# Kernel optimization log

Hardware: AMD Instinct MI355X
Metric: run time of the kernel (lower is better)

The kernel has to match this reference:

```python
import jax, jax.numpy as jnp
import numpy as np

B, N, M = 8, 4096, 4096
CHAMFER_W, EMD_W, UNC_W = 1.0, 0.5, 0.01


def setup_inputs() -> dict:
    key = jax.random.key(0)
    k1, k2, k3 = jax.random.split(key, 3)
    return {
        "pred_pc": jax.random.normal(k1, (B, N, 3), dtype=jnp.float32),
        "target_pc": jax.random.normal(k2, (B, M, 3), dtype=jnp.float32),
        "uncertainty": jax.random.uniform(k3, (B, N), dtype=jnp.float32),
    }


def reference(pred_pc, target_pc, uncertainty):
    # squared pairwise distances via ||p||^2 + ||t||^2 - 2 p.t  -> [B, N, M]
    pred_sq = jnp.sum(pred_pc ** 2, axis=2, keepdims=True)            # [B, N, 1]
    tgt_sq = jnp.sum(target_pc ** 2, axis=2, keepdims=True)           # [B, M, 1]
    cross = jnp.einsum('bnd,bmd->bnm', pred_pc, target_pc)            # [B, N, M]
    d2 = pred_sq + jnp.swapaxes(tgt_sq, 1, 2) - 2.0 * cross           # [B, N, M]

    # ChamferDistanceLoss: mean of min squared dists both directions
    chamfer = jnp.mean(jnp.min(d2, axis=2)) + jnp.mean(jnp.min(d2, axis=1))

    # EMDLoss: torch.cdist p=2 (euclidean), min over targets, mean
    dist = jnp.sqrt(jnp.clip(d2, 0.0))
    emd = jnp.mean(jnp.min(dist, axis=2))

    # uncertainty regularizer
    unc_reg = jnp.mean(uncertainty) * UNC_W

    total = chamfer * CHAMFER_W + emd * EMD_W + unc_reg
    return total
```

## Files before the change

kernel.cpp:

```cpp
#include <hip/hip_runtime.h>
#include <math.h>

typedef _Float16 half8  __attribute__((ext_vector_type(8)));
typedef float    f32x16 __attribute__((ext_vector_type(16)));

#define Bb 8
#define Nn 4096
#define Mm 4096
#define BLOCK 256
#define WAVES 4
#define NTA 2
#define QBLK 256
#define TBLK 1024
#define MT (TBLK / 32)
#define MS 4
#define QTILES (Nn / QBLK)
#define NQ (2 * Bb * Nn)

template<int CTRL>
__device__ __forceinline__ float dppmin(float v) {
    int iv = __float_as_int(v);
    iv = __builtin_amdgcn_update_dpp(iv, iv, CTRL, 0xF, 0xF, false);
    return fminf(v, __int_as_float(iv));
}
__device__ __forceinline__ float rowmin32(float v) {
    v = dppmin<0xB1>(v);
    v = dppmin<0x4E>(v);
    v = dppmin<0x141>(v);
    v = dppmin<0x140>(v);
    v = fminf(v, __shfl_xor(v, 16));
    return v;
}


__global__ void __launch_bounds__(BLOCK) chamfer_mfma32_kernel(
    const float* __restrict__ pred,
    const float* __restrict__ targ,
    float* __restrict__ mins)
{
    __shared__ uint4 fragB[TBLK];

    const int tid  = threadIdx.x;
    const int lane = tid & 63;
    const int wave = tid >> 6;

    const int id  = blockIdx.x;
    const int ms  = id & 3;
    const int qt  = (id >> 2) & 15;
    const int b   = (id >> 6) & 7;
    const int dir = id >> 9;

    const float* Q = dir ? targ : pred;
    const float* T = dir ? pred : targ;

    for (int s = tid; s < TBLK; s += BLOCK) {
        const float* gp = T + ((size_t)b * Mm + ms * TBLK + s) * 3;
        _Float16 xh = (_Float16)gp[0], yh = (_Float16)gp[1], zh = (_Float16)gp[2];
        float xq = (float)xh, yq = (float)yh, zq = (float)zh;
        float tt = fmaf(xq, xq, fmaf(yq, yq, zq * zq));
        _Float16 th = (_Float16)tt;
        _Float16 tl = (_Float16)(tt - (float)th);
        const _Float16 m2 = (_Float16)(-2.0f);
        half8 h;
        h[0] = m2 * xh; h[1] = m2 * yh; h[2] = m2 * zh; h[3] = (_Float16)1.0f;
        h[4] = th; h[5] = (_Float16)1.0f; h[6] = tl; h[7] = (_Float16)0.0f;
        fragB[s] = *reinterpret_cast<uint4*>(&h);
    }

    const int qbase = qt * QBLK + wave * (NTA * 32);
    half8 a0, a1;
    #pragma unroll
    for (int e = 0; e < 8; ++e) { a0[e] = (_Float16)0.0f; a1[e] = (_Float16)0.0f; }
    if (lane < 32) {
        #pragma unroll
        for (int t = 0; t < NTA; ++t) {
            const int n = qbase + t * 32 + lane;
            const float* gp = Q + ((size_t)b * Nn + n) * 3;
            _Float16 xh = (_Float16)gp[0], yh = (_Float16)gp[1], zh = (_Float16)gp[2];
            float xq = (float)xh, yq = (float)yh, zq = (float)zh;
            float pp = fmaf(xq, xq, fmaf(yq, yq, zq * zq));
            _Float16 ph = (_Float16)pp;
            _Float16 pl = (_Float16)(pp - (float)ph);
            half8 h;
            h[0] = xh; h[1] = yh; h[2] = zh; h[3] = ph;
            h[4] = (_Float16)1.0f; h[5] = pl; h[6] = (_Float16)1.0f; h[7] = (_Float16)0.0f;
            if (t == 0) a0 = h; else a1 = h;
        }
    }
    __syncthreads();

    const int col = lane & 31;
    const f32x16 cz = {};
    const float inf = __builtin_inff();
    f32x16 acc0, acc1;
    #pragma unroll
    for (int k = 0; k < 16; ++k) { acc0[k] = inf; acc1[k] = inf; }

    for (int j = 0; j < MT; j += 2) {
        half8 b0 = *reinterpret_cast<const half8*>(&fragB[(j << 5) + col]);
        half8 b1 = *reinterpret_cast<const half8*>(&fragB[((j + 1) << 5) + col]);
        f32x16 c0 = __builtin_amdgcn_mfma_f32_32x32x16_f16(a0, b0, cz, 0, 0, 0);
        f32x16 c1 = __builtin_amdgcn_mfma_f32_32x32x16_f16(a0, b1, cz, 0, 0, 0);
        #pragma unroll
        for (int k = 0; k < 16; ++k)
            acc0[k] = fminf(fminf(acc0[k], c0[k]), c1[k]);
        f32x16 d0 = __builtin_amdgcn_mfma_f32_32x32x16_f16(a1, b0, cz, 0, 0, 0);
        f32x16 d1 = __builtin_amdgcn_mfma_f32_32x32x16_f16(a1, b1, cz, 0, 0, 0);
        #pragma unroll
        for (int k = 0; k < 16; ++k)
            acc1[k] = fminf(fminf(acc1[k], d0[k]), d1[k]);
    }

    const int hi = lane >> 5;
    const size_t qoff = ((size_t)dir * Bb + b) * Nn;
    #pragma unroll
    for (int r = 0; r < 16; ++r) {
        float v0 = rowmin32(acc0[r]);
        float v1 = rowmin32(acc1[r]);
        if (col == 0) {
            const int rl = (r & 3) + 8 * (r >> 2) + 4 * hi;
            const size_t q0 = qoff + qbase + rl;
            mins[q0 * MS + ms]        = v0;
            mins[(q0 + 32) * MS + ms] = v1;
        }
    }
}

__global__ void __launch_bounds__(256) reduce_kernel(
    const float* __restrict__ mins, const float* __restrict__ unc,
    float* __restrict__ partials)
{
    const int q = blockIdx.x * 256 + threadIdx.x;
    const float4* m4 = (const float4*)mins;

    float4 a4 = m4[q];
    float4 b4 = m4[q + 32768];
    float vA = fminf(fminf(a4.x, a4.y), fminf(a4.z, a4.w));
    float vB = fminf(fminf(b4.x, b4.y), fminf(b4.z, b4.w));
    float sA = vA, sE = sqrtf(fmaxf(vA, 0.f)), sB = vB, sU = unc[q];

    #pragma unroll
    for (int off = 32; off > 0; off >>= 1) {
        sA += __shfl_down(sA, off);  sE += __shfl_down(sE, off);
        sB += __shfl_down(sB, off);  sU += __shfl_down(sU, off);
    }
    __shared__ float sw[4][4];
    const int lane = threadIdx.x & 63, wave = threadIdx.x >> 6;
    if (lane == 0) { sw[wave][0] = sA; sw[wave][1] = sE;
                     sw[wave][2] = sB; sw[wave][3] = sU; }
    __syncthreads();
    if (threadIdx.x < 4) {
        partials[blockIdx.x * 4 + threadIdx.x] =
            sw[0][threadIdx.x] + sw[1][threadIdx.x] +
            sw[2][threadIdx.x] + sw[3][threadIdx.x];
    }
}

__global__ void __launch_bounds__(64) finalize_kernel(
    const float* __restrict__ partials, float* __restrict__ out)
{
    const float4* p4 = (const float4*)partials;
    float4 s0 = p4[threadIdx.x], s1 = p4[threadIdx.x + 64];
    float sA = s0.x + s1.x, sE = s0.y + s1.y, sB = s0.z + s1.z, sU = s0.w + s1.w;
    #pragma unroll
    for (int off = 32; off > 0; off >>= 1) {
        sA += __shfl_down(sA, off);  sE += __shfl_down(sE, off);
        sB += __shfl_down(sB, off);  sU += __shfl_down(sU, off);
    }
    if (threadIdx.x == 0) {
        const float invBN = 1.0f / (float)(Bb * Nn);
        const float invBM = 1.0f / (float)(Bb * Mm);
        out[0] = (sA * invBN + sB * invBM) + 0.5f * (sE * invBN)
               + 0.01f * (sU * invBN);
    }
}

extern "C" void kernel_launch(void* const* d_in, const int* in_sizes, int n_in,
                              void* d_out, int out_size, void* d_ws, size_t ws_size,
                              hipStream_t stream) {
    const float* pred = (const float*)d_in[0];
    const float* targ = (const float*)d_in[1];
    const float* unc  = (const float*)d_in[2];
    float* out      = (float*)d_out;
    float* mins     = (float*)d_ws;
    float* partials = (float*)d_ws + (size_t)NQ * MS;

    chamfer_mfma32_kernel<<<1024, BLOCK, 0, stream>>>(pred, targ, mins);
    reduce_kernel<<<128, 256, 0, stream>>>(mins, unc, partials);
    finalize_kernel<<<1, 64, 0, stream>>>(partials, out);
}
```

Measured before the change: 25.93 us.

## Fuse chamfer min, reduction and finalize into one kernel with last-block reduction

Result: faster. 25.31 us (-2.4%).

```diff
diff --git a/kernel.cpp b/kernel.cpp
--- a/kernel.cpp
+++ b/kernel.cpp
@@ -7,15 +7,10 @@
 #define Bb 8
 #define Nn 4096
 #define Mm 4096
-#define BLOCK 256
-#define WAVES 4
-#define NTA 2
-#define QBLK 256
-#define TBLK 1024
-#define MT (TBLK / 32)
-#define MS 4
-#define QTILES (Nn / QBLK)
-#define NQ (2 * Bb * Nn)
+#define BLOCK 512
+#define QBLK 128
+#define NQT (Nn / QBLK)
+#define GRID 512
 
 template<int CTRL>
 __device__ __forceinline__ float dppmin(float v) {
@@ -32,29 +27,35 @@
     return v;
 }
 
-
-__global__ void __launch_bounds__(BLOCK) chamfer_mfma32_kernel(
+__global__ void __launch_bounds__(BLOCK, 4) chamfer_onepass_kernel(
     const float* __restrict__ pred,
     const float* __restrict__ targ,
-    float* __restrict__ mins)
+    const float* __restrict__ unc,
+    float4* __restrict__ psum,
+    unsigned* __restrict__ fcnt,
+    float* __restrict__ out)
 {
-    __shared__ uint4 fragB[TBLK];
+    __shared__ uint4 fragB[Mm];
+    __shared__ float smin[QBLK * 4];
+    __shared__ float wsum[32];
+    __shared__ int   sflag;
 
     const int tid  = threadIdx.x;
     const int lane = tid & 63;
     const int wave = tid >> 6;
+    const int qhalf = wave >> 2;
+    const int mslot = wave & 3;
 
     const int id  = blockIdx.x;
-    const int ms  = id & 3;
-    const int qt  = (id >> 2) & 15;
-    const int b   = (id >> 6) & 7;
-    const int dir = id >> 9;
+    const int qt  = id & 31;
+    const int b   = (id >> 5) & 7;
+    const int dir = id >> 8;
 
     const float* Q = dir ? targ : pred;
     const float* T = dir ? pred : targ;
 
-    for (int s = tid; s < TBLK; s += BLOCK) {
-        const float* gp = T + ((size_t)b * Mm + ms * TBLK + s) * 3;
+    for (int s = tid; s < Mm; s += BLOCK) {
+        const float* gp = T + ((size_t)b * Mm + s) * 3;
         _Float16 xh = (_Float16)gp[0], yh = (_Float16)gp[1], zh = (_Float16)gp[2];
         float xq = (float)xh, yq = (float)yh, zq = (float)zh;
         float tt = fmaf(xq, xq, fmaf(yq, yq, zq * zq));
@@ -67,13 +68,13 @@
         fragB[s] = *reinterpret_cast<uint4*>(&h);
     }
 
-    const int qbase = qt * QBLK + wave * (NTA * 32);
+    const int qbase = qt * QBLK + qhalf * 64;
     half8 a0, a1;
     #pragma unroll
     for (int e = 0; e < 8; ++e) { a0[e] = (_Float16)0.0f; a1[e] = (_Float16)0.0f; }
     if (lane < 32) {
         #pragma unroll
-        for (int t = 0; t < NTA; ++t) {
+        for (int t = 0; t < 2; ++t) {
             const int n = qbase + t * 32 + lane;
             const float* gp = Q + ((size_t)b * Nn + n) * 3;
             _Float16 xh = (_Float16)gp[0], yh = (_Float16)gp[1], zh = (_Float16)gp[2];
@@ -96,7 +97,9 @@
     #pragma unroll
     for (int k = 0; k < 16; ++k) { acc0[k] = inf; acc1[k] = inf; }
 
-    for (int j = 0; j < MT; j += 2) {
+    const int jbase = mslot * 32;
+    for (int jj = 0; jj < 32; jj += 2) {
+        const int j = jbase + jj;
         half8 b0 = *reinterpret_cast<const half8*>(&fragB[(j << 5) + col]);
         half8 b1 = *reinterpret_cast<const half8*>(&fragB[((j + 1) << 5) + col]);
         f32x16 c0 = __builtin_amdgcn_mfma_f32_32x32x16_f16(a0, b0, cz, 0, 0, 0);
@@ -112,66 +115,80 @@
     }
 
     const int hi = lane >> 5;
-    const size_t qoff = ((size_t)dir * Bb + b) * Nn;
     #pragma unroll
     for (int r = 0; r < 16; ++r) {
         float v0 = rowmin32(acc0[r]);
         float v1 = rowmin32(acc1[r]);
         if (col == 0) {
             const int rl = (r & 3) + 8 * (r >> 2) + 4 * hi;
-            const size_t q0 = qoff + qbase + rl;
-            mins[q0 * MS + ms]        = v0;
-            mins[(q0 + 32) * MS + ms] = v1;
-        }
-    }
-}
-
-__global__ void __launch_bounds__(256) reduce_kernel(
-    const float* __restrict__ mins, const float* __restrict__ unc,
-    float* __restrict__ partials)
-{
-    const int q = blockIdx.x * 256 + threadIdx.x;
-    const float4* m4 = (const float4*)mins;
-
-    float4 a4 = m4[q];
-    float4 b4 = m4[q + 32768];
-    float vA = fminf(fminf(a4.x, a4.y), fminf(a4.z, a4.w));
-    float vB = fminf(fminf(b4.x, b4.y), fminf(b4.z, b4.w));
-    float sA = vA, sE = sqrtf(fmaxf(vA, 0.f)), sB = vB, sU = unc[q];
-
-    #pragma unroll
-    for (int off = 32; off > 0; off >>= 1) {
-        sA += __shfl_down(sA, off);  sE += __shfl_down(sE, off);
-        sB += __shfl_down(sB, off);  sU += __shfl_down(sU, off);
-    }
-    __shared__ float sw[4][4];
-    const int lane = threadIdx.x & 63, wave = threadIdx.x >> 6;
-    if (lane == 0) { sw[wave][0] = sA; sw[wave][1] = sE;
-                     sw[wave][2] = sB; sw[wave][3] = sU; }
-    __syncthreads();
-    if (threadIdx.x < 4) {
-        partials[blockIdx.x * 4 + threadIdx.x] =
-            sw[0][threadIdx.x] + sw[1][threadIdx.x] +
-            sw[2][threadIdx.x] + sw[3][threadIdx.x];
-    }
-}
-
-__global__ void __launch_bounds__(64) finalize_kernel(
-    const float* __restrict__ partials, float* __restrict__ out)
-{
-    const float4* p4 = (const float4*)partials;
-    float4 s0 = p4[threadIdx.x], s1 = p4[threadIdx.x + 64];
-    float sA = s0.x + s1.x, sE = s0.y + s1.y, sB = s0.z + s1.z, sU = s0.w + s1.w;
-    #pragma unroll
-    for (int off = 32; off > 0; off >>= 1) {
-        sA += __shfl_down(sA, off);  sE += __shfl_down(sE, off);
-        sB += __shfl_down(sB, off);  sU += __shfl_down(sU, off);
-    }
-    if (threadIdx.x == 0) {
-        const float invBN = 1.0f / (float)(Bb * Nn);
-        const float invBM = 1.0f / (float)(Bb * Mm);
-        out[0] = (sA * invBN + sB * invBM) + 0.5f * (sE * invBN)
-               + 0.01f * (sU * invBN);
+            smin[(qhalf * 64 + rl) * 4 + mslot]      = v0;
+            smin[(qhalf * 64 + 32 + rl) * 4 + mslot] = v1;
+        }
+    }
+    __syncthreads();
+
+    float s1 = 0.f, s2 = 0.f, su = 0.f;
+    if (tid < QBLK) {
+        const float4 m = ((const float4*)smin)[tid];
+        const float d2 = fminf(fminf(m.x, m.y), fminf(m.z, m.w));
+        s1 = d2;
+        s2 = dir ? 0.f : sqrtf(fmaxf(d2, 0.f));
+    }
+    if (tid < 64) su = unc[id * 64 + tid];
+    #pragma unroll
+    for (int m = 1; m < 64; m <<= 1) {
+        s1 += __shfl_xor(s1, m);
+        s2 += __shfl_xor(s2, m);
+        su += __shfl_xor(su, m);
+    }
+    if (lane == 0) {
+        wsum[wave * 4 + 0] = s1;
+        wsum[wave * 4 + 1] = s2;
+        wsum[wave * 4 + 2] = su;
+    }
+    __syncthreads();
+
+    if (tid == 0) {
+        float S1 = 0.f, S2 = 0.f, SU = 0.f;
+        #pragma unroll
+        for (int w = 0; w < 8; ++w) {
+            S1 += wsum[w * 4 + 0]; S2 += wsum[w * 4 + 1]; SU += wsum[w * 4 + 2];
+        }
+        psum[id] = make_float4(S1, S2, SU, 0.f);
+        __threadfence();
+        unsigned old = atomicAdd(fcnt, 1u);
+        sflag = (((old + 1) & (GRID - 1)) == 0) ? 1 : 0;
+    }
+    __syncthreads();
+
+    if (sflag) {
+        __threadfence();
+        const float4 v = psum[tid];
+        float sa = (tid < GRID / 2) ? v.x : 0.f;
+        float sb = (tid < GRID / 2) ? 0.f : v.x;
+        float se = v.y;
+        float s3 = v.z;
+        #pragma unroll
+        for (int m = 1; m < 64; m <<= 1) {
+            sa += __shfl_xor(sa, m); sb += __shfl_xor(sb, m);
+            se += __shfl_xor(se, m); s3 += __shfl_xor(s3, m);
+        }
+        __syncthreads();
+        if (lane == 0) {
+            wsum[wave * 4 + 0] = sa; wsum[wave * 4 + 1] = sb;
+            wsum[wave * 4 + 2] = se; wsum[wave * 4 + 3] = s3;
+        }
+        __syncthreads();
+        if (tid == 0) {
+            float SA = 0.f, SB = 0.f, SE = 0.f, SU = 0.f;
+            #pragma unroll
+            for (int w = 0; w < 8; ++w) {
+                SA += wsum[w * 4 + 0]; SB += wsum[w * 4 + 1];
+                SE += wsum[w * 4 + 2]; SU += wsum[w * 4 + 3];
+            }
+            const float inv = 1.0f / (float)(Bb * Nn);
+            out[0] = (SA + SB) * inv + 0.5f * SE * inv + 0.01f * SU * inv;
+        }
     }
 }
 
@@ -181,11 +198,11 @@
     const float* pred = (const float*)d_in[0];
     const float* targ = (const float*)d_in[1];
     const float* unc  = (const float*)d_in[2];
-    float* out      = (float*)d_out;
-    float* mins     = (float*)d_ws;
-    float* partials = (float*)d_ws + (size_t)NQ * MS;
-
-    chamfer_mfma32_kernel<<<1024, BLOCK, 0, stream>>>(pred, targ, mins);
-    reduce_kernel<<<128, 256, 0, stream>>>(mins, unc, partials);
-    finalize_kernel<<<1, 64, 0, stream>>>(partials, out);
-}
+    float* out = (float*)d_out;
+
+    float4*   psum = (float4*)d_ws;
+    unsigned* fcnt = (unsigned*)((char*)d_ws + 8192);
+
+    chamfer_onepass_kernel<<<GRID, BLOCK, 0, stream>>>(pred, targ, unc,
+                                                       psum, fcnt, out);
+}
```
